# Performance work log

Hardware: AMD Instinct MI355X
Metric: run time of the kernel (lower is better)

The kernel has to match this reference:

```python
import jax, jax.numpy as jnp
import numpy as np
from jax import lax

B, H, W, C = 2, 256, 256, 192
HEADS = 6
WS = 8                      # window size
PW = WS // 2                # permuted window size (kv downsampled 2x2)
HIDDEN = 4 * C
HEAD_DIM = C // HEADS
SCALE = HEAD_DIM ** -0.5
N_WIN = WS * WS             # 64 query tokens per window
N_KV = PW * PW              # 16 kv tokens per window


def _aligned_index(pw0, pw1):
    ch = np.arange(pw0)
    cw = np.arange(pw1)
    coords = np.stack(np.meshgrid(ch, cw, indexing='ij'))          # (2, pw0, pw1)
    cf = coords.reshape(2, -1)
    rel = (cf[:, :, None] - cf[:, None, :]).transpose(1, 2, 0).astype(np.int64)
    rel[:, :, 0] += pw0 - 1
    rel[:, :, 1] += pw1 - 1
    rel[:, :, 0] *= 2 * pw1 - 1
    idx = rel.sum(-1)                                              # (N_KV, N_KV)
    n4 = pw0 * pw1
    idx = idx.reshape(pw0, pw1, 1, 1, n4)
    idx = np.tile(idx, (1, 1, 2, 2, 1)).transpose(0, 2, 1, 3, 4).reshape(4 * n4, n4)
    return jnp.asarray(idx)

IDX = _aligned_index(PW, PW)   # (N_WIN, N_KV)


def layernorm(x, g, b):
    mu = x.mean(-1, keepdims=True)
    var = ((x - mu) ** 2).mean(-1, keepdims=True)
    return (x - mu) * lax.rsqrt(var + 1e-5) * g + b


def window_partition(x):
    # (B, H, W, C) -> (B*nW, WS, WS, C)
    x = x.reshape(B, H // WS, WS, W // WS, WS, C)
    return x.transpose(0, 1, 3, 2, 4, 5).reshape(-1, WS, WS, C)


def window_reverse(w):
    # (B*nW, WS, WS, C) -> (B, H, W, C)
    x = w.reshape(B, H // WS, W // WS, WS, WS, C)
    return x.transpose(0, 1, 3, 2, 4, 5).reshape(B, H, W, C)


def setup_inputs() -> dict:
    key = jax.random.key(0)
    ks = jax.random.split(key, 10)
    rn = lambda k, shp, s=0.02: jax.random.normal(k, shp, jnp.float32) * s
    return {
        'x': jax.random.normal(ks[0], (B, H * W, C), jnp.float32),
        'g1': jnp.ones((C,), jnp.float32), 'be1': jnp.zeros((C,), jnp.float32),
        'wq': rn(ks[1], (C, C)), 'bq': jnp.zeros((C,), jnp.float32),
        'wkv': rn(ks[2], (C, C // 2)), 'bkv': jnp.zeros((C // 2,), jnp.float32),
        'bias_table': rn(ks[3], ((2 * PW - 1) * (2 * PW - 1), HEADS)),
        'wproj': rn(ks[4], (C, C)), 'bproj': jnp.zeros((C,), jnp.float32),
        'g2': jnp.ones((C,), jnp.float32), 'be2': jnp.zeros((C,), jnp.float32),
        'w1f': rn(ks[5], (C, HIDDEN)), 'b1f': jnp.zeros((HIDDEN,), jnp.float32),
        'dwk': rn(ks[6], (HIDDEN, 1, 5, 5)), 'dwb': jnp.zeros((HIDDEN,), jnp.float32),
        'w2f': rn(ks[7], (HIDDEN, C)), 'b2f': jnp.zeros((C,), jnp.float32),
    }


def reference(x, g1, be1, wq, bq, wkv, bkv, bias_table, wproj, bproj,
              g2, be2, w1f, b1f, dwk, dwb, w2f, b2f):
    shortcut = x
    xn = layernorm(x, g1, be1).reshape(B, H, W, C)
    xw = window_partition(xn).reshape(-1, N_WIN, C)        # (b_, 64, C)
    b_ = xw.shape[0]
    # PSA: kv downsampled 2x2 spatially, 2x2 block folded into channels
    kv = (xw @ wkv + bkv).reshape(b_, PW, 2, PW, 2, 2, C // 4)
    kv = kv.transpose(0, 1, 3, 5, 2, 4, 6).reshape(b_, N_KV, 2, HEADS, HEAD_DIM)
    kv = kv.transpose(2, 0, 3, 1, 4)                       # (2, b_, h, N_KV, d)
    k, v = kv[0], kv[1]
    q = (xw @ wq + bq).reshape(b_, N_WIN, HEADS, HEAD_DIM).transpose(0, 2, 1, 3) * SCALE
    attn = jnp.einsum('bhqd,bhkd->bhqk', q, k)             # (b_, h, 64, 16)
    bias = bias_table[IDX.reshape(-1)].reshape(N_WIN, N_KV, HEADS).transpose(2, 0, 1)
    attn = jax.nn.softmax(attn + bias[None], axis=-1)
    aw = jnp.einsum('bhqk,bhkd->bhqd', attn, v).transpose(0, 2, 1, 3).reshape(b_, N_WIN, C)
    aw = aw @ wproj + bproj
    x = shortcut + window_reverse(aw.reshape(-1, WS, WS, C)).reshape(B, H * W, C)
    # ConvFFN with depthwise-conv residual branch
    xn2 = layernorm(x, g2, be2)
    h1 = jax.nn.gelu(xn2 @ w1f + b1f, approximate=False)   # (B, HW, HIDDEN)
    img = h1.transpose(0, 2, 1).reshape(B, HIDDEN, H, W)
    conv = lax.conv_general_dilated(img, dwk, (1, 1), ((2, 2), (2, 2)),
                                    feature_group_count=HIDDEN,
                                    dimension_numbers=('NCHW', 'OIHW', 'NCHW'))
    conv = jax.nn.gelu(conv + dwb[None, :, None, None], approximate=False)
    h = h1 + conv.reshape(B, HIDDEN, H * W).transpose(0, 2, 1)
    return x + (h @ w2f + b2f)
```

## Files before the change

kernel.cpp:

```cpp
#include <hip/hip_runtime.h>
#include <hip/hip_bf16.h>
#include <math.h>

#define NTOK  131072
#define NTOKH 65536
#define CD    192
#define HID   768

typedef short bf16x8 __attribute__((ext_vector_type(8)));
typedef float f32x4  __attribute__((ext_vector_type(4)));

__device__ __forceinline__ float bf2f(unsigned short v) {
    union { unsigned int u; float f; } c; c.u = ((unsigned int)v) << 16; return c.f;
}
__device__ __forceinline__ unsigned short f2bf(float f) {
    __hip_bfloat16 h = __float2bfloat16(f);
    return *reinterpret_cast<unsigned short*>(&h);
}
__device__ __forceinline__ float gelu_f(float x) {
    return 0.5f * x * (1.0f + erff(x * 0.7071067811865476f));
}

__device__ __forceinline__ void gld16(const unsigned short* g, unsigned short* l) {
    __builtin_amdgcn_global_load_lds(
        (const __attribute__((address_space(1))) void*)(unsigned long long)(g),
        (__attribute__((address_space(3))) void*)(unsigned int)(unsigned long long)(l),
        16, 0, 0);
}

__global__ __launch_bounds__(256) void ln_kernel(const float* __restrict__ x,
                                                 const float* __restrict__ g,
                                                 const float* __restrict__ b,
                                                 unsigned short* __restrict__ out) {
    int tok  = blockIdx.x * 4 + (threadIdx.x >> 6);
    int lane = threadIdx.x & 63;
    const float* xp = x + (size_t)tok * CD;
    float v0 = xp[lane], v1 = xp[lane + 64], v2 = xp[lane + 128];
    float s  = v0 + v1 + v2;
    float s2 = v0 * v0 + v1 * v1 + v2 * v2;
    #pragma unroll
    for (int off = 32; off > 0; off >>= 1) {
        s  += __shfl_xor(s,  off, 64);
        s2 += __shfl_xor(s2, off, 64);
    }
    float mu  = s * (1.0f / 192.0f);
    float var = s2 * (1.0f / 192.0f) - mu * mu;
    float rs  = rsqrtf(var + 1e-5f);
    unsigned short* op = out + (size_t)tok * CD;
    op[lane]       = f2bf((v0 - mu) * rs * g[lane]       + b[lane]);
    op[lane + 64]  = f2bf((v1 - mu) * rs * g[lane + 64]  + b[lane + 64]);
    op[lane + 128] = f2bf((v2 - mu) * rs * g[lane + 128] + b[lane + 128]);
}

__global__ __launch_bounds__(256) void wconv_kernel(
    const float* __restrict__ wq, const float* __restrict__ wkv,
    const float* __restrict__ wproj, const float* __restrict__ w1f,
    const float* __restrict__ w2f,
    unsigned short* __restrict__ qkvT, unsigned short* __restrict__ projT,
    unsigned short* __restrict__ w1T, unsigned short* __restrict__ w2T)
{
    int i = blockIdx.x * 256 + threadIdx.x;
    if (i < 288 * 192) {
        int n = i / 192, k = i - n * 192;
        float v = (n < 192) ? wq[(size_t)k * 192 + n] : wkv[(size_t)k * 96 + (n - 192)];
        qkvT[n * 192 + k] = f2bf(v);
    }
    if (i < 192 * 192) {
        int n = i / 192, k = i - n * 192;
        projT[n * 192 + k] = f2bf(wproj[(size_t)k * 192 + n]);
    }
    {
        int n = i / 192, k = i - n * 192;
        w1T[n * 192 + k] = f2bf(w1f[(size_t)k * 768 + n]);
    }
    {
        int n = i / 768, k = i - n * 768;
        w2T[n * 768 + k] = f2bf(w2f[(size_t)k * 192 + n]);
    }
}

template<int MODE>
__global__ __launch_bounds__(256) void mgemm_kernel(
    const unsigned short* __restrict__ A,
    const unsigned short* __restrict__ WT,
    const float* __restrict__ b0, const float* __restrict__ b1,
    const float* __restrict__ addsrc,
    void* O0, unsigned short* __restrict__ O1,
    int K, int Nreal)
{
    constexpr int BM = 128, BN = 96, BK = 64;
    __shared__ unsigned short As[BM * BK];
    __shared__ unsigned short Bs[BN * BK];
    const int tid  = threadIdx.x;
    const int wave = tid >> 6, lane = tid & 63;
    const int quad = lane >> 4, l16 = lane & 15;
    const int wm = (wave >> 1) * 64, wn = (wave & 1) * 48;
    const int m0 = blockIdx.y * BM, n0 = blockIdx.x * BN;

    f32x4 acc[4][3];
    #pragma unroll
    for (int mi = 0; mi < 4; mi++)
        #pragma unroll
        for (int ni = 0; ni < 3; ni++) acc[mi][ni] = (f32x4){0.f, 0.f, 0.f, 0.f};

    const int r8 = lane >> 3;
    const int sw = ((lane & 7) ^ r8) << 3;
    const unsigned short* aSrc = A  + (size_t)(m0 + wave * 32 + r8) * K + sw;
    const unsigned short* bSrc = WT + (size_t)(n0 + wave * 24 + r8) * K + sw;
    unsigned short* aDst = &As[(wave * 32) * BK];
    unsigned short* bDst = &Bs[(wave * 24) * BK];

    for (int k0 = 0; k0 < K; k0 += BK) {
        #pragma unroll
        for (int i = 0; i < 4; i++)
            gld16(aSrc + k0 + i * 8 * K, aDst + i * 8 * BK);
        #pragma unroll
        for (int i = 0; i < 3; i++)
            gld16(bSrc + k0 + i * 8 * K, bDst + i * 8 * BK);
        __syncthreads();

        #pragma unroll
        for (int kk = 0; kk < 2; kk++) {
            const int cb = kk * 64 + quad * 16;
            bf16x8 bfr[3];
            #pragma unroll
            for (int ni = 0; ni < 3; ni++) {
                int br = wn + ni * 16 + l16;
                bfr[ni] = *(const bf16x8*)&Bs[br * BK + ((cb ^ ((br & 7) << 4)) >> 1)];
            }
            #pragma unroll
            for (int mi = 0; mi < 4; mi++) {
                int ar = wm + mi * 16 + l16;
                bf16x8 af = *(const bf16x8*)&As[ar * BK + ((cb ^ ((ar & 7) << 4)) >> 1)];
                acc[mi][0] = __builtin_amdgcn_mfma_f32_16x16x32_bf16(af, bfr[0], acc[mi][0], 0, 0, 0);
                acc[mi][1] = __builtin_amdgcn_mfma_f32_16x16x32_bf16(af, bfr[1], acc[mi][1], 0, 0, 0);
                acc[mi][2] = __builtin_amdgcn_mfma_f32_16x16x32_bf16(af, bfr[2], acc[mi][2], 0, 0, 0);
            }
        }
        __syncthreads();
    }

    #pragma unroll
    for (int mi = 0; mi < 4; mi++) {
        int row0 = m0 + wm + mi * 16 + quad * 4;
        #pragma unroll
        for (int ni = 0; ni < 3; ni++) {
            int col = n0 + wn + ni * 16 + l16;
            #pragma unroll
            for (int r = 0; r < 4; r++) {
                size_t m = (size_t)(row0 + r);
                float v = acc[mi][ni][r];
                if (MODE == 0) {
                    if (col < 192)
                        ((unsigned short*)O0)[m * 192 + col] =
                            f2bf((v + b0[col]) * 0.17677669529663687f);
                    else
                        O1[m * 96 + (col - 192)] = f2bf(v + b1[col - 192]);
                } else if (MODE == 1) {
                    ((float*)O0)[m * 192 + col] = v + b0[col] + addsrc[m * 192 + col];
                } else if (MODE == 2) {
                    ((unsigned short*)O0)[m * 768 + col] = f2bf(gelu_f(v + b0[col]));
                } else {
                    float* op = (float*)O0;
                    op[m * 192 + col] = op[m * 192 + col] + v + b0[col];
                }
            }
        }
    }
}

__global__ __launch_bounds__(384) void attn_kernel(
    const unsigned short* __restrict__ q, const unsigned short* __restrict__ kvp,
    const float* __restrict__ bt, unsigned short* __restrict__ aw)
{
    __shared__ float ks[6][16][32];
    __shared__ float vs[6][16][32];
    const int w = blockIdx.x;
    const int b = w >> 10, rem = w & 1023, wh = rem >> 5, wc = rem & 31;
    const int tid = threadIdx.x;
    const size_t base = (size_t)b * 65536;

    for (int e = tid; e < 16 * 192; e += 384) {
        int kk = e / 192, f = e - kk * 192;
        int d1 = kk >> 2, d3 = kk & 3;
        int d2 = f / 96;  int r = f - d2 * 96;
        int d4 = r / 48;  int c4 = r - d4 * 48;
        int i = 2 * d1 + d2, j = 2 * d3 + d4;
        size_t g = base + (size_t)(wh * 8 + i) * 256 + (wc * 8 + j);
        int h = f >> 5, d = f & 31;
        ks[h][kk][d] = bf2f(kvp[g * 96 + c4]);
        vs[h][kk][d] = bf2f(kvp[g * 96 + 48 + c4]);
    }
    __syncthreads();

    const int t = tid & 63, h = tid >> 6;
    const int i = t >> 3, j = t & 7;
    const int iq2 = i >> 1, jq2 = j >> 1;
    const size_t g = base + (size_t)(wh * 8 + i) * 256 + (wc * 8 + j);

    float qr[32];
    const ushort4* qp = (const ushort4*)(q + g * 192 + h * 32);
    #pragma unroll
    for (int d4i = 0; d4i < 8; d4i++) {
        ushort4 u = qp[d4i];
        qr[d4i * 4 + 0] = bf2f(u.x); qr[d4i * 4 + 1] = bf2f(u.y);
        qr[d4i * 4 + 2] = bf2f(u.z); qr[d4i * 4 + 3] = bf2f(u.w);
    }

    float lg[16]; float mx = -1e30f;
    #pragma unroll
    for (int kk = 0; kk < 16; kk++) {
        int kh = kk >> 2, kw = kk & 3;
        float s = bt[((iq2 - kh + 3) * 7 + (jq2 - kw + 3)) * 6 + h];
        #pragma unroll
        for (int d = 0; d < 32; d++) s = fmaf(qr[d], ks[h][kk][d], s);
        lg[kk] = s; mx = fmaxf(mx, s);
    }
    float den = 0.f;
    #pragma unroll
    for (int kk = 0; kk < 16; kk++) { lg[kk] = expf(lg[kk] - mx); den += lg[kk]; }
    float inv = 1.0f / den;

    float oacc[32];
    #pragma unroll
    for (int d = 0; d < 32; d++) oacc[d] = 0.f;
    #pragma unroll
    for (int kk = 0; kk < 16; kk++) {
        float p = lg[kk] * inv;
        #pragma unroll
        for (int d = 0; d < 32; d++) oacc[d] = fmaf(p, vs[h][kk][d], oacc[d]);
    }
    unsigned short* op = aw + g * 192 + h * 32;
    #pragma unroll
    for (int d = 0; d < 32; d++) op[d] = f2bf(oacc[d]);
}

__global__ __launch_bounds__(256) void dwconv_kernel(
    const unsigned short* __restrict__ h1,
    const float* __restrict__ dwk, const float* __restrict__ dwb,
    unsigned short* __restrict__ hout)
{
    __shared__ float tile[12][12][64];
    int bx = blockIdx.x;
    int chb = bx % 12; int t = bx / 12;
    int tw = t % 32; int th = t / 32;
    const int tid = threadIdx.x;
    const int chbase = chb * 64;
    const int ch = tid & 63;
    const int cp = tid >> 6;
    const int c0 = cp * 2;

    float w[25];
    #pragma unroll
    for (int tap = 0; tap < 25; tap++)
        w[tap] = dwk[(size_t)(chbase + ch) * 25 + tap];
    const float bias = dwb[chbase + ch];

    const int lane4 = tid & 15;
    const int pg = tid >> 4;
    for (int p = pg; p < 144; p += 16) {
        int pr = p / 12, pc = p - pr * 12;
        int r = th * 8 - 2 + pr, c = tw * 8 - 2 + pc;
        float f0 = 0.f, f1 = 0.f, f2 = 0.f, f3 = 0.f;
        if (r >= 0 && r < 256 && c >= 0 && c < 256) {
            const unsigned short* sp = h1 + (((size_t)r * 256 + c) * HID + chbase + lane4 * 4);
            ushort4 u = *(const ushort4*)sp;
            f0 = bf2f(u.x); f1 = bf2f(u.y); f2 = bf2f(u.z); f3 = bf2f(u.w);
        }
        tile[pr][pc][lane4 * 4 + 0] = f0;
        tile[pr][pc][lane4 * 4 + 1] = f1;
        tile[pr][pc][lane4 * 4 + 2] = f2;
        tile[pr][pc][lane4 * 4 + 3] = f3;
    }
    __syncthreads();

    float win[5][6];
    #pragma unroll
    for (int rr = 0; rr < 4; rr++)
        #pragma unroll
        for (int cc = 0; cc < 6; cc++)
            win[rr][cc] = tile[rr][c0 + cc][ch];

    #pragma unroll
    for (int r0 = 0; r0 < 8; r0++) {
        #pragma unroll
        for (int cc = 0; cc < 6; cc++)
            win[(r0 + 4) % 5][cc] = tile[r0 + 4][c0 + cc][ch];
        float s0 = bias, s1 = bias;
        #pragma unroll
        for (int kr = 0; kr < 5; kr++) {
            int ri = (r0 + kr) % 5;
            #pragma unroll
            for (int kc = 0; kc < 5; kc++) {
                float wt = w[kr * 5 + kc];
                s0 = fmaf(win[ri][kc],     wt, s0);
                s1 = fmaf(win[ri][kc + 1], wt, s1);
            }
        }
        float v0 = win[(r0 + 2) % 5][2] + gelu_f(s0);
        float v1 = win[(r0 + 2) % 5][3] + gelu_f(s1);
        size_t tok = (size_t)(th * 8 + r0) * 256 + tw * 8 + c0;
        hout[tok * HID + chbase + ch]         = f2bf(v0);
        hout[(tok + 1) * HID + chbase + ch]   = f2bf(v1);
    }
}

extern "C" void kernel_launch(void* const* d_in, const int* in_sizes, int n_in,
                              void* d_out, int out_size, void* d_ws, size_t ws_size,
                              hipStream_t stream) {
    const float* x    = (const float*)d_in[0];
    const float* g1   = (const float*)d_in[1];
    const float* be1  = (const float*)d_in[2];
    const float* wq   = (const float*)d_in[3];
    const float* bq   = (const float*)d_in[4];
    const float* wkv  = (const float*)d_in[5];
    const float* bkv  = (const float*)d_in[6];
    const float* btab = (const float*)d_in[7];
    const float* wproj= (const float*)d_in[8];
    const float* bproj= (const float*)d_in[9];
    const float* g2   = (const float*)d_in[10];
    const float* be2  = (const float*)d_in[11];
    const float* w1f  = (const float*)d_in[12];
    const float* b1f  = (const float*)d_in[13];
    const float* dwk  = (const float*)d_in[14];
    const float* dwb  = (const float*)d_in[15];
    const float* w2f  = (const float*)d_in[16];
    const float* b2f  = (const float*)d_in[17];
    float* out = (float*)d_out;

    char* ws = (char*)d_ws;
    unsigned short* xnb  = (unsigned short*)(ws);
    unsigned short* qb   = (unsigned short*)(ws + 50331648);
    unsigned short* kvb  = (unsigned short*)(ws + 100663296);
    unsigned short* h1b  = (unsigned short*)(ws + 125829120);
    unsigned short* hhb  = (unsigned short*)(ws + 226492416);
    unsigned short* qkvT = (unsigned short*)(ws + 327155712);
    unsigned short* projT= (unsigned short*)(ws + 327266304);
    unsigned short* w1T  = (unsigned short*)(ws + 327340032);
    unsigned short* w2T  = (unsigned short*)(ws + 327634944);

    wconv_kernel<<<576, 256, 0, stream>>>(wq, wkv, wproj, w1f, w2f,
                                          qkvT, projT, w1T, w2T);
    ln_kernel<<<NTOK / 4, 256, 0, stream>>>(x, g1, be1, xnb);
    mgemm_kernel<0><<<dim3(3, NTOK / 128), 256, 0, stream>>>(
        xnb, qkvT, bq, bkv, nullptr, qb, kvb, 192, 288);
    attn_kernel<<<2048, 384, 0, stream>>>(qb, kvb, btab, xnb);
    mgemm_kernel<1><<<dim3(2, NTOK / 128), 256, 0, stream>>>(
        xnb, projT, bproj, nullptr, x, out, nullptr, 192, 192);
    ln_kernel<<<NTOK / 4, 256, 0, stream>>>(out, g2, be2, qb);
    for (int half = 0; half < 2; half++) {
        const unsigned short* xn2h = qb + (size_t)half * NTOKH * CD;
        float* outh = out + (size_t)half * NTOKH * CD;
        mgemm_kernel<2><<<dim3(8, NTOKH / 128), 256, 0, stream>>>(
            xn2h, w1T, b1f, nullptr, nullptr, h1b, nullptr, 192, 768);
        dwconv_kernel<<<12 * 32 * 32, 256, 0, stream>>>(h1b, dwk, dwb, hhb);
        mgemm_kernel<3><<<dim3(2, NTOKH / 128), 256, 0, stream>>>(
            hhb, w2T, b2f, nullptr, nullptr, outh, nullptr, 768, 192);
    }
}
```

Before: 804.3 us.

## Add XCD block swizzle, packed FMA in attention/dwconv, cheaper epilogues

Remaps GEMM workgroup IDs so consecutive tiles land on the same XCD for better L2 reuse. Hoists bias loads out of the GEMM epilogue and uses 32-bit index arithmetic. Attention and depthwise conv switch to float2 packed FMA (v_pk_fma_f32), and attention output is written as packed 32-bit pairs. bf16 rounding is replaced with a manual round-to-nearest-even bit trick that does not handle NaN.

```diff
diff --git a/kernel.cpp b/kernel.cpp
--- a/kernel.cpp
+++ b/kernel.cpp
@@ -9,13 +9,15 @@
 
 typedef short bf16x8 __attribute__((ext_vector_type(8)));
 typedef float f32x4  __attribute__((ext_vector_type(4)));
+typedef float f32x2  __attribute__((ext_vector_type(2)));
 
 __device__ __forceinline__ float bf2f(unsigned short v) {
     union { unsigned int u; float f; } c; c.u = ((unsigned int)v) << 16; return c.f;
 }
 __device__ __forceinline__ unsigned short f2bf(float f) {
-    __hip_bfloat16 h = __float2bfloat16(f);
-    return *reinterpret_cast<unsigned short*>(&h);
+    union { float f; unsigned int u; } c; c.f = f;
+    unsigned int r = c.u + 0x7FFFu + ((c.u >> 16) & 1u);
+    return (unsigned short)(r >> 16);
 }
 __device__ __forceinline__ float gelu_f(float x) {
     return 0.5f * x * (1.0f + erff(x * 0.7071067811865476f));
@@ -77,6 +79,15 @@
         int n = i / 768, k = i - n * 768;
         w2T[n * 768 + k] = f2bf(w2f[(size_t)k * 192 + n]);
     }
+}
+
+__device__ __forceinline__ void xcd_swz(int gx, int& bx, int& by) {
+    int nwg  = gx * (int)gridDim.y;
+    int id   = (int)blockIdx.y * gx + (int)blockIdx.x;
+    int q    = nwg >> 3, r = nwg & 7;
+    int xcd  = id & 7, rest = id >> 3;
+    int sw   = (xcd < r ? xcd * (q + 1) : r * (q + 1) + (xcd - r) * q) + rest;
+    bx = sw % gx; by = sw / gx;
 }
 
 template<int MODE>
@@ -95,7 +106,8 @@
     const int wave = tid >> 6, lane = tid & 63;
     const int quad = lane >> 4, l16 = lane & 15;
     const int wm = (wave >> 1) * 64, wn = (wave & 1) * 48;
-    const int m0 = blockIdx.y * BM, n0 = blockIdx.x * BN;
+    int bx, by; xcd_swz(gridDim.x, bx, by);
+    const int m0 = by * BM, n0 = bx * BN;
 
     f32x4 acc[4][3];
     #pragma unroll
@@ -140,30 +152,54 @@
         __syncthreads();
     }
 
+    float bc[3], bc1[3];
+    #pragma unroll
+    for (int ni = 0; ni < 3; ni++) {
+        int col = n0 + wn + ni * 16 + l16;
+        if (MODE == 0) {
+            if (n0 < 192) bc[ni] = b0[col];
+            else          bc1[ni] = b1[col - 192];
+        } else {
+            bc[ni] = b0[col];
+        }
+    }
     #pragma unroll
     for (int mi = 0; mi < 4; mi++) {
         int row0 = m0 + wm + mi * 16 + quad * 4;
         #pragma unroll
-        for (int ni = 0; ni < 3; ni++) {
-            int col = n0 + wn + ni * 16 + l16;
-            #pragma unroll
-            for (int r = 0; r < 4; r++) {
-                size_t m = (size_t)(row0 + r);
-                float v = acc[mi][ni][r];
-                if (MODE == 0) {
-                    if (col < 192)
-                        ((unsigned short*)O0)[m * 192 + col] =
-                            f2bf((v + b0[col]) * 0.17677669529663687f);
-                    else
-                        O1[m * 96 + (col - 192)] = f2bf(v + b1[col - 192]);
-                } else if (MODE == 1) {
-                    ((float*)O0)[m * 192 + col] = v + b0[col] + addsrc[m * 192 + col];
-                } else if (MODE == 2) {
-                    ((unsigned short*)O0)[m * 768 + col] = f2bf(gelu_f(v + b0[col]));
+        for (int r = 0; r < 4; r++) {
+            unsigned mrow = (unsigned)(row0 + r);
+            if (MODE == 0) {
+                if (n0 < 192) {
+                    unsigned ob = mrow * 192u + (unsigned)(n0 + wn + l16);
+                    unsigned short* q0 = (unsigned short*)O0;
+                    #pragma unroll
+                    for (int ni = 0; ni < 3; ni++)
+                        q0[ob + ni * 16] = f2bf((acc[mi][ni][r] + bc[ni]) * 0.17677669529663687f);
                 } else {
-                    float* op = (float*)O0;
-                    op[m * 192 + col] = op[m * 192 + col] + v + b0[col];
+                    unsigned ob = mrow * 96u + (unsigned)(n0 - 192 + wn + l16);
+                    #pragma unroll
+                    for (int ni = 0; ni < 3; ni++)
+                        O1[ob + ni * 16] = f2bf(acc[mi][ni][r] + bc1[ni]);
                 }
+            } else if (MODE == 1) {
+                unsigned ob = mrow * 192u + (unsigned)(n0 + wn + l16);
+                float* op = (float*)O0;
+                #pragma unroll
+                for (int ni = 0; ni < 3; ni++)
+                    op[ob + ni * 16] = acc[mi][ni][r] + bc[ni] + addsrc[ob + ni * 16];
+            } else if (MODE == 2) {
+                unsigned ob = mrow * 768u + (unsigned)(n0 + wn + l16);
+                unsigned short* op = (unsigned short*)O0;
+                #pragma unroll
+                for (int ni = 0; ni < 3; ni++)
+                    op[ob + ni * 16] = f2bf(gelu_f(acc[mi][ni][r] + bc[ni]));
+            } else {
+                unsigned ob = mrow * 192u + (unsigned)(n0 + wn + l16);
+                float* op = (float*)O0;
+                #pragma unroll
+                for (int ni = 0; ni < 3; ni++)
+                    op[ob + ni * 16] = op[ob + ni * 16] + acc[mi][ni][r] + bc[ni];
             }
         }
     }
@@ -198,22 +234,24 @@
     const int iq2 = i >> 1, jq2 = j >> 1;
     const size_t g = base + (size_t)(wh * 8 + i) * 256 + (wc * 8 + j);
 
-    float qr[32];
+    f32x2 qr[16];
     const ushort4* qp = (const ushort4*)(q + g * 192 + h * 32);
     #pragma unroll
     for (int d4i = 0; d4i < 8; d4i++) {
         ushort4 u = qp[d4i];
-        qr[d4i * 4 + 0] = bf2f(u.x); qr[d4i * 4 + 1] = bf2f(u.y);
-        qr[d4i * 4 + 2] = bf2f(u.z); qr[d4i * 4 + 3] = bf2f(u.w);
+        qr[d4i * 2 + 0] = (f32x2){bf2f(u.x), bf2f(u.y)};
+        qr[d4i * 2 + 1] = (f32x2){bf2f(u.z), bf2f(u.w)};
     }
 
     float lg[16]; float mx = -1e30f;
     #pragma unroll
     for (int kk = 0; kk < 16; kk++) {
         int kh = kk >> 2, kw = kk & 3;
-        float s = bt[((iq2 - kh + 3) * 7 + (jq2 - kw + 3)) * 6 + h];
-        #pragma unroll
-        for (int d = 0; d < 32; d++) s = fmaf(qr[d], ks[h][kk][d], s);
+        const f32x2* kp = (const f32x2*)&ks[h][kk][0];
+        f32x2 a2 = (f32x2){bt[((iq2 - kh + 3) * 7 + (jq2 - kw + 3)) * 6 + h], 0.f};
+        #pragma unroll
+        for (int d = 0; d < 16; d++) a2 = __builtin_elementwise_fma(qr[d], kp[d], a2);
+        float s = a2.x + a2.y;
         lg[kk] = s; mx = fmaxf(mx, s);
     }
     float den = 0.f;
@@ -221,18 +259,23 @@
     for (int kk = 0; kk < 16; kk++) { lg[kk] = expf(lg[kk] - mx); den += lg[kk]; }
     float inv = 1.0f / den;
 
-    float oacc[32];
-    #pragma unroll
-    for (int d = 0; d < 32; d++) oacc[d] = 0.f;
+    f32x2 oacc[16];
+    #pragma unroll
+    for (int d = 0; d < 16; d++) oacc[d] = (f32x2){0.f, 0.f};
     #pragma unroll
     for (int kk = 0; kk < 16; kk++) {
         float p = lg[kk] * inv;
-        #pragma unroll
-        for (int d = 0; d < 32; d++) oacc[d] = fmaf(p, vs[h][kk][d], oacc[d]);
-    }
-    unsigned short* op = aw + g * 192 + h * 32;
-    #pragma unroll
-    for (int d = 0; d < 32; d++) op[d] = f2bf(oacc[d]);
+        f32x2 pv = (f32x2){p, p};
+        const f32x2* vp = (const f32x2*)&vs[h][kk][0];
+        #pragma unroll
+        for (int d = 0; d < 16; d++) oacc[d] = __builtin_elementwise_fma(pv, vp[d], oacc[d]);
+    }
+    unsigned int* op = (unsigned int*)(aw + g * 192 + h * 32);
+    #pragma unroll
+    for (int d = 0; d < 16; d++) {
+        unsigned int lo = f2bf(oacc[d].x), hi = f2bf(oacc[d].y);
+        op[d] = lo | (hi << 16);
+    }
 }
 
 __global__ __launch_bounds__(256) void dwconv_kernel(
@@ -274,34 +317,39 @@
     }
     __syncthreads();
 
-    float win[5][6];
+    f32x2 a[5][5];
     #pragma unroll
     for (int rr = 0; rr < 4; rr++)
         #pragma unroll
-        for (int cc = 0; cc < 6; cc++)
-            win[rr][cc] = tile[rr][c0 + cc][ch];
+        for (int kc = 0; kc < 5; kc++)
+            a[rr][kc] = (f32x2){tile[rr][c0 + kc][ch], tile[rr][c0 + kc + 1][ch]};
+
+    unsigned obase = ((unsigned)(th * 8) * 256u + (unsigned)(tw * 8 + c0)) * (unsigned)HID
+                   + (unsigned)(chbase + ch);
 
     #pragma unroll
     for (int r0 = 0; r0 < 8; r0++) {
-        #pragma unroll
-        for (int cc = 0; cc < 6; cc++)
-            win[(r0 + 4) % 5][cc] = tile[r0 + 4][c0 + cc][ch];
-        float s0 = bias, s1 = bias;
+        const int rn = (r0 + 4) % 5;
+        #pragma unroll
+        for (int kc = 0; kc < 5; kc++)
+            a[rn][kc] = (f32x2){tile[r0 + 4][c0 + kc][ch], tile[r0 + 4][c0 + kc + 1][ch]};
+
+        f32x2 s = (f32x2){bias, bias};
         #pragma unroll
         for (int kr = 0; kr < 5; kr++) {
-            int ri = (r0 + kr) % 5;
+            const int ri = (r0 + kr) % 5;
             #pragma unroll
             for (int kc = 0; kc < 5; kc++) {
                 float wt = w[kr * 5 + kc];
-                s0 = fmaf(win[ri][kc],     wt, s0);
-                s1 = fmaf(win[ri][kc + 1], wt, s1);
+                s = __builtin_elementwise_fma((f32x2){wt, wt}, a[ri][kc], s);
             }
         }
-        float v0 = win[(r0 + 2) % 5][2] + gelu_f(s0);
-        float v1 = win[(r0 + 2) % 5][3] + gelu_f(s1);
-        size_t tok = (size_t)(th * 8 + r0) * 256 + tw * 8 + c0;
-        hout[tok * HID + chbase + ch]         = f2bf(v0);
-        hout[(tok + 1) * HID + chbase + ch]   = f2bf(v1);
+        const int rc = (r0 + 2) % 5;
+        float v0 = a[rc][2].x + gelu_f(s.x);
+        float v1 = a[rc][2].y + gelu_f(s.y);
+        hout[obase]       = f2bf(v0);
+        hout[obase + HID] = f2bf(v1);
+        obase += 256u * (unsigned)HID;
     }
 }
 
```

Result: no change. 804.4 us (+0.0%).
